# Kernel tuning notes

Hardware: AMD Instinct MI355X
Metric: run time of the kernel (lower is better)

## Reference

```python
import jax, jax.numpy as jnp
import numpy as np

H, C = 33, 16  # heads, out_channels (concat=False -> mean over heads)
NEG_SLOPE = 0.2


def setup_inputs() -> dict:
    key = jax.random.key(0)
    ks = jax.random.split(key, 6)
    N, E, F_in = 50000, 320000, 128
    x = jax.random.normal(ks[0], (N, F_in), dtype=jnp.float32)
    edge_index = jax.random.randint(ks[1], (2, E), 0, N, dtype=jnp.int64)
    W = jax.random.normal(ks[2], (F_in, H * C), dtype=jnp.float32) * (1.0 / np.sqrt(F_in))
    att_src = jax.random.normal(ks[3], (H, C), dtype=jnp.float32) * 0.1
    att_dst = jax.random.normal(ks[4], (H, C), dtype=jnp.float32) * 0.1
    bias = jnp.zeros((C,), dtype=jnp.float32)
    return {"x": x, "edge_index": edge_index, "W": W, "att_src": att_src, "att_dst": att_dst, "bias": bias}


def reference(x, edge_index, W, att_src, att_dst, bias):
    N = x.shape[0]
    # add self loops (PyG GATConv default add_self_loops=True)
    loop = jnp.arange(N, dtype=edge_index.dtype)
    src = jnp.concatenate([edge_index[0], loop])  # [Et]
    dst = jnp.concatenate([edge_index[1], loop])  # [Et]

    h = (x @ W).reshape(N, H, C)                       # [N,H,C]
    a_src = jnp.einsum('nhc,hc->nh', h, att_src)       # [N,H]
    a_dst = jnp.einsum('nhc,hc->nh', h, att_dst)       # [N,H]

    e = a_src[src] + a_dst[dst]                        # [Et,H]
    e = jnp.where(e > 0, e, NEG_SLOPE * e)             # leaky_relu

    # segment softmax over incoming edges of each destination node
    m = jax.ops.segment_max(e, dst, num_segments=N)    # [N,H]
    ex = jnp.exp(e - m[dst])                           # [Et,H]
    denom = jax.ops.segment_sum(ex, dst, num_segments=N)  # [N,H]
    alpha = ex / (denom[dst] + 1e-16)                  # [Et,H]

    msg = alpha[:, :, None] * h[src]                   # [Et,H,C]
    out = jax.ops.segment_sum(msg, dst, num_segments=N)  # [N,H,C]
    out = out.mean(axis=1) + bias                      # concat=False -> mean heads
    return jnp.tanh(out)
```

## Files before the change

kernel.cpp:

```cpp
#include <hip/hip_runtime.h>
#include <math.h>

#define H_HEADS 33
#define C_CH    16
#define HC      528
#define JG      11
#define JGT     13
#define F_IN    128
#define NEG_SLOPE 0.2f

#define BSH   7
#define BMAX  1024
#define PCH   4096

typedef short  bf16x8  __attribute__((ext_vector_type(8)));
typedef float  floatx4 __attribute__((ext_vector_type(4)));

__device__ inline unsigned short f2bf(float f) {
    unsigned int u = __float_as_uint(f);
    unsigned int r = u + 0x7fffu + ((u >> 16) & 1u);
    return (unsigned short)(r >> 16);
}
__device__ inline float bflo(unsigned int u) {
    return __uint_as_float(u << 16);
}
__device__ inline float bfhi(unsigned int u) {
    return __uint_as_float(u & 0xffff0000u);
}

__device__ inline void load_edges4(const int* __restrict__ ei, int E, int Et,
                                   int e0, int* src, int* dst)
{
    if (e0 + 3 < E) {
        int4 s4 = *(const int4*)&ei[e0];
        src[0] = s4.x; src[1] = s4.y; src[2] = s4.z; src[3] = s4.w;
        if ((E & 3) == 0) {
            int4 d4 = *(const int4*)&ei[E + e0];
            dst[0] = d4.x; dst[1] = d4.y; dst[2] = d4.z; dst[3] = d4.w;
        } else {
            #pragma unroll
            for (int k = 0; k < 4; ++k) dst[k] = ei[E + e0 + k];
        }
    } else {
        #pragma unroll
        for (int k = 0; k < 4; ++k) {
            int g = e0 + k;
            if (g < E)       { src[k] = ei[g]; dst[k] = ei[E + g]; }
            else if (g < Et) { src[k] = dst[k] = g - E; }
            else             { src[k] = dst[k] = -1; }
        }
    }
}

#define PW1 (F_IN * HC)
#define PW2 (PW1 + 96 * F_IN)
__global__ void prep_kernel(const float* __restrict__ W,
                            const float* __restrict__ att_src,
                            const float* __restrict__ att_dst,
                            unsigned short* __restrict__ Wt,
                            float4* __restrict__ zout, int nzo,
                            int4* __restrict__ zb, int nzb)
{
    int g = blockIdx.x * blockDim.x + threadIdx.x;
    if (g < PW1) {
        int k = g / HC, n = g % HC;
        Wt[n * F_IN + k] = f2bf(W[g]);
    } else if (g < PW2) {
        int gg = g - PW1;
        int nl = gg >> 7, k = gg & 127;
        int grp = nl / 48, h = nl % 48;
        float v = 0.f;
        if (h < H_HEADS) {
            const float* att = grp ? att_dst : att_src;
            const float* wr  = W + (size_t)k * HC + h * C_CH;
            #pragma unroll
            for (int c = 0; c < C_CH; ++c) v += wr[c] * att[h * C_CH + c];
        }
        Wt[(size_t)(HC + nl) * F_IN + k] = f2bf(v);
    } else {
        int z = g - PW2;
        if (z < nzo)            zout[z]     = make_float4(0.f, 0.f, 0.f, 0.f);
        else if (z - nzo < nzb) zb[z - nzo] = make_int4(0, 0, 0, 0);
    }
}

#define LDA 136
__global__ __launch_bounds__(256) void gemm_att_kernel(
    const float* __restrict__ x, const unsigned short* __restrict__ Wt,
    unsigned short* __restrict__ hb,
    float* __restrict__ a_src, float* __restrict__ a_dstc, int N)
{
    __shared__ unsigned short U[64 * LDA];
    unsigned short (*As)[LDA] = (unsigned short (*)[LDA])U;
    unsigned short (*Bs)[LDA] = (unsigned short (*)[LDA])U;

    const int tid  = threadIdx.x;
    const int lane = tid & 63;
    const int wave = tid >> 6;
    const int lm   = lane & 15;
    const int kc   = lane >> 4;
    const int m0   = blockIdx.x * 64;
    const size_t segN = (size_t)N * 48;

    for (int e = tid; e < 64 * 32; e += 256) {
        int r = e >> 5, c = e & 31;
        int gr = m0 + r;
        float4 v = (gr < N) ? ((const float4*)(x + (size_t)gr * F_IN))[c]
                            : make_float4(0.f, 0.f, 0.f, 0.f);
        unsigned int lo = (unsigned int)f2bf(v.x) | ((unsigned int)f2bf(v.y) << 16);
        unsigned int hi = (unsigned int)f2bf(v.z) | ((unsigned int)f2bf(v.w) << 16);
        *(uint2*)&As[r][c * 4] = make_uint2(lo, hi);
    }

    const uint4* wp = (const uint4*)Wt;
    uint4 rb0 = wp[tid], rb1 = wp[tid + 256], rb2 = wp[tid + 512];

    __syncthreads();

    const int arow = wave * 16 + lm;
    bf16x8 afrag[4];
    #pragma unroll
    for (int ks = 0; ks < 4; ++ks)
        afrag[ks] = *(const bf16x8*)&As[arow][ks * 32 + kc * 8];

    #pragma unroll 1
    for (int j = 0; j < JGT; ++j) {
        __syncthreads();
        *(uint4*)&Bs[tid >> 4][(tid & 15) * 8] = rb0;
        { int e = tid + 256; *(uint4*)&Bs[e >> 4][(e & 15) * 8] = rb1; }
        { int e = tid + 512; *(uint4*)&Bs[e >> 4][(e & 15) * 8] = rb2; }
        if (j + 1 < JGT) {
            int b = (j + 1) * 768;
            rb0 = wp[b + tid]; rb1 = wp[b + tid + 256]; rb2 = wp[b + tid + 512];
        }
        __syncthreads();

        floatx4 acc[3] = {};
        #pragma unroll
        for (int ks = 0; ks < 4; ++ks) {
            #pragma unroll
            for (int t = 0; t < 3; ++t) {
                bf16x8 b = *(const bf16x8*)&Bs[t * 16 + lm][ks * 32 + kc * 8];
                acc[t] = __builtin_amdgcn_mfma_f32_16x16x32_bf16(afrag[ks], b, acc[t], 0, 0, 0);
            }
        }

        #pragma unroll
        for (int t = 0; t < 3; ++t) {
            #pragma unroll
            for (int rr = 0; rr < 4; ++rr) {
                const int row = m0 + wave * 16 + kc * 4 + rr;
                if (row >= N) continue;
                if (j < JG) {
                    hb[(size_t)j * segN + (size_t)row * 48 + t * 16 + lm] =
                        f2bf(acc[t][rr]);
                } else {
                    const int col = t * 16 + lm;
                    if (col < H_HEADS) {
                        float* dstp = (j == JG) ? a_src : a_dstc;
                        dstp[(size_t)row * H_HEADS + col] = acc[t][rr];
                    }
                }
            }
        }
    }
}

__global__ __launch_bounds__(256) void bhist_kernel(const int* __restrict__ ei,
                                                    int* __restrict__ bhist,
                                                    int E, int Et)
{
    __shared__ int lh[2 * BMAX];
    const int tid = threadIdx.x;
    for (int i = tid; i < 2 * BMAX; i += 256) lh[i] = 0;
    __syncthreads();
    int e0 = (blockIdx.x * 256 + tid) * 8;
    if (e0 < Et) {
        int s4[4], d4[4];
        #pragma unroll
        for (int h = 0; h < 2; ++h) {
            load_edges4(ei, E, Et, e0 + h * 4, s4, d4);
            #pragma unroll
            for (int k = 0; k < 4; ++k)
                if (s4[k] >= 0) {
                    atomicAdd(&lh[s4[k] >> BSH], 1);
                    atomicAdd(&lh[BMAX + (d4[k] >> BSH)], 1);
                }
        }
    }
    __syncthreads();
    for (int i = tid; i < 2 * BMAX; i += 256) {
        int v = lh[i];
        if (v) atomicAdd(&bhist[i], v);
    }
}

__global__ __launch_bounds__(1024) void scanb_kernel(const int* __restrict__ bhist,
                                                     int* __restrict__ bbase,
                                                     int* __restrict__ cursor,
                                                     int nb)
{
    const int side = blockIdx.x;
    const int tid  = threadIdx.x;
    const int* h = bhist + side * BMAX;
    int* bb  = bbase  + side * (BMAX + 1);
    int* cur = cursor + side * BMAX;
    __shared__ int sa[1024];
    int v = (tid < nb) ? h[tid] : 0;
    sa[tid] = v;
    __syncthreads();
    for (int off = 1; off < 1024; off <<= 1) {
        int t = (tid >= off) ? sa[tid - off] : 0;
        __syncthreads();
        sa[tid] += t;
        __syncthreads();
    }
    int incl = sa[tid];
    if (tid < nb) {
        bb[tid]  = incl - v;
        cur[tid] = incl - v;
        if (tid == nb - 1) bb[nb] = incl;
    }
}

__global__ __launch_bounds__(256) void part_kernel(const int* __restrict__ ei,
                                                   int* __restrict__ cursor,
                                                   int2* __restrict__ Ag,
                                                   int E, int Et)
{
    __shared__ int2 kv[PCH];
    __shared__ int  lhist[512];
    __shared__ int  gbias[512];
    __shared__ int  wsum[4];
    __shared__ int  sTot;

    const int side = blockIdx.y;
    const int tid  = threadIdx.x;
    const int lane = tid & 63, wid = tid >> 6;
    for (int i = tid; i < 512; i += 256) lhist[i] = 0;
    __syncthreads();

    const int c0 = blockIdx.x * PCH;
    int2 kvr[16];
    #pragma unroll
    for (int r = 0; r < 4; ++r) {
        int e0 = c0 + r * 1024 + tid * 4;
        int s4[4], d4[4];
        load_edges4(ei, E, Et, e0, s4, d4);
        #pragma unroll
        for (int k = 0; k < 4; ++k) {
            int key = side ? d4[k] : s4[k];
            int val = side ? s4[k] : d4[k];
            kvr[r * 4 + k] = make_int2(key, val);
            if (key >= 0) atomicAdd(&lhist[key >> BSH], 1);
        }
    }
    __syncthreads();

    int a0 = lhist[2 * tid], a1 = lhist[2 * tid + 1];
    int pair = a0 + a1, s = pair;
    #pragma unroll
    for (int d = 1; d < 64; d <<= 1) {
        int t = __shfl_up(s, d);
        if (lane >= d) s += t;
    }
    if (lane == 63) wsum[wid] = s;
    __syncthreads();
    if (tid == 0) {
        int run = 0;
        #pragma unroll
        for (int i = 0; i < 4; ++i) { int t = wsum[i]; wsum[i] = run; run += t; }
    }
    __syncthreads();
    int exclT = s - pair + wsum[wid];
    int e0x = exclT, e1x = exclT + a0;
    if (tid == 255) sTot = e1x + a1;
    lhist[2 * tid]     = e0x;
    lhist[2 * tid + 1] = e1x;
    if (a0 > 0) {
        int gb = atomicAdd(&cursor[side * BMAX + 2 * tid], a0);
        gbias[2 * tid] = gb - e0x;
    }
    if (a1 > 0) {
        int gb = atomicAdd(&cursor[side * BMAX + 2 * tid + 1], a1);
        gbias[2 * tid + 1] = gb - e1x;
    }
    __syncthreads();

    #pragma unroll
    for (int k = 0; k < 16; ++k) {
        int key = kvr[k].x;
        if (key >= 0) {
            int lp = atomicAdd(&lhist[key >> BSH], 1);
            kv[lp] = kvr[k];
        }
    }
    __syncthreads();

    const int tot = sTot;
    for (int i = tid; i < tot; i += 256) {
        int2 e = kv[i];
        int b = e.x >> BSH;
        Ag[(size_t)side * Et + gbias[b] + i] = e;
    }
}

__global__ __launch_bounds__(256) void p2_kernel(const int2* __restrict__ Ag,
                                                 const int* __restrict__ bbase,
                                                 int2* __restrict__ e2,
                                                 int* __restrict__ ss2,
                                                 int* __restrict__ off_d,
                                                 int N, int Et, int nb)
{
    const int side = blockIdx.y;
    const int b    = blockIdx.x;
    if (b >= nb) return;
    const int tid  = threadIdx.x;
    const int base = bbase[side * (BMAX + 1) + b];
    const int end  = bbase[side * (BMAX + 1) + b + 1];
    const int k0   = b << BSH;
    const int2* A  = Ag + (size_t)side * Et;

    __shared__ int lh[128];
    __shared__ int w0;
    if (tid < 128) lh[tid] = 0;
    __syncthreads();
    for (int i = base + tid; i < end; i += 256)
        atomicAdd(&lh[A[i].x - k0], 1);
    __syncthreads();

    int v = 0, s = 0;
    if (tid < 128) {
        v = lh[tid]; s = v;
        #pragma unroll
        for (int d = 1; d < 64; d <<= 1) {
            int t = __shfl_up(s, d);
            if ((tid & 63) >= d) s += t;
        }
    }
    if (tid == 63) w0 = s;
    __syncthreads();
    if (tid >= 64 && tid < 128) s += w0;
    int start = base + s - v;
    if (tid < 128) {
        lh[tid] = start;
        if (side == 1 && (k0 + tid) < N) off_d[k0 + tid] = start;
    }
    __syncthreads();

    for (int i = base + tid; i < end; i += 256) {
        int2 e = A[i];
        int pos = atomicAdd(&lh[e.x - k0], 1);
        if (side == 0) e2[pos] = e;
        else           ss2[pos] = e.y;
    }
}

__global__ __launch_bounds__(256) void denom_kernel(
    const int* __restrict__ off_d, const int* __restrict__ ss2,
    const float* __restrict__ a_src, const float* __restrict__ a_dstc,
    float* __restrict__ ad2, int N, int Et)
{
    int g = blockIdx.x * blockDim.x + threadIdx.x;
    if (g >= N * H_HEADS) return;
    const int d = g / H_HEADS, h = g - d * H_HEADS;
    const int beg = off_d[d];
    const int end = (d + 1 < N) ? off_d[d + 1] : Et;
    const float ad = a_dstc[g];
    float acc = 0.f;
    int e = beg;
    for (; e + 4 <= end; e += 4) {
        int s0 = ss2[e], s1 = ss2[e + 1], s2 = ss2[e + 2], s3 = ss2[e + 3];
        float v0 = a_src[(size_t)s0 * H_HEADS + h];
        float v1 = a_src[(size_t)s1 * H_HEADS + h];
        float v2 = a_src[(size_t)s2 * H_HEADS + h];
        float v3 = a_src[(size_t)s3 * H_HEADS + h];
        v0 += ad; v0 = v0 > 0.f ? v0 : NEG_SLOPE * v0;
        v1 += ad; v1 = v1 > 0.f ? v1 : NEG_SLOPE * v1;
        v2 += ad; v2 = v2 > 0.f ? v2 : NEG_SLOPE * v2;
        v3 += ad; v3 = v3 > 0.f ? v3 : NEG_SLOPE * v3;
        acc += __expf(v0);
        acc += __expf(v1);
        acc += __expf(v2);
        acc += __expf(v3);
    }
    for (; e < end; ++e) {
        float v = a_src[(size_t)ss2[e] * H_HEADS + h] + ad;
        v = v > 0.f ? v : NEG_SLOPE * v;
        acc += __expf(v);
    }
    ((float2*)ad2)[g] = make_float2(ad, 1.0f / (acc + 1e-16f));
}

#define EPB 64
__global__ __launch_bounds__(256, 4) void aggregate_kernel(
    const int2* __restrict__ e2,
    const float* __restrict__ a_src, const float* __restrict__ ad2,
    const unsigned short* __restrict__ hb,
    float* __restrict__ out, int N, int Et)
{
    __shared__ int   s_src[EPB], s_dst[EPB];
    __shared__ float s_alpha[EPB][H_HEADS];

    const int nwg = gridDim.x;
    const int q = nwg >> 3, r = nwg & 7;
    const int xcd = blockIdx.x & 7, idx = blockIdx.x >> 3;
    const int bid = (xcd < r ? xcd * (q + 1) : r * (q + 1) + (xcd - r) * q) + idx;

    const int tid = threadIdx.x;
    const int e0  = bid * EPB;
    const size_t segN = (size_t)N * 48;

    if (tid < EPB) {
        int e = e0 + tid;
        int2 v = (e < Et) ? e2[e] : make_int2(0, 0);
        s_src[tid] = v.x; s_dst[tid] = v.y;
    }
    __syncthreads();

    float2 di[9]; float as[9];
    #pragma unroll
    for (int rr = 0; rr < 8; ++rr) {
        int i = tid + rr * 256;
        int el = i / H_HEADS, hd = i - el * H_HEADS;
        di[rr] = ((const float2*)ad2)[(size_t)s_dst[el] * H_HEADS + hd];
        as[rr] = a_src[(size_t)s_src[el] * H_HEADS + hd];
    }
    if (tid < 64) {
        int i = 2048 + tid;
        int el = i / H_HEADS, hd = i - el * H_HEADS;
        di[8] = ((const float2*)ad2)[(size_t)s_dst[el] * H_HEADS + hd];
        as[8] = a_src[(size_t)s_src[el] * H_HEADS + hd];
    }
    __builtin_amdgcn_sched_barrier(0);
    #pragma unroll
    for (int rr = 0; rr < 8; ++rr) {
        int i = tid + rr * 256;
        int el = i / H_HEADS, hd = i - el * H_HEADS;
        float v = as[rr] + di[rr].x;
        v = v > 0.f ? v : NEG_SLOPE * v;
        s_alpha[el][hd] = __expf(v) * di[rr].y;
    }
    if (tid < 64) {
        int i = 2048 + tid;
        int el = i / H_HEADS, hd = i - el * H_HEADS;
        float v = as[8] + di[8].x;
        v = v > 0.f ? v : NEG_SLOPE * v;
        s_alpha[el][hd] = __expf(v) * di[8].y;
    }
    __syncthreads();

    const int el = tid >> 2, cq = tid & 3;
    const int src = s_src[el];
    const unsigned short* hp = hb + (size_t)src * 48 + cq * 4;
    uint2 w[33];
    #pragma unroll
    for (int j = 0; j < JG; ++j) {
        const unsigned short* pj = hp + (size_t)j * segN;
        w[3 * j + 0] = *(const uint2*)(pj);
        w[3 * j + 1] = *(const uint2*)(pj + 16);
        w[3 * j + 2] = *(const uint2*)(pj + 32);
    }
    __builtin_amdgcn_sched_barrier(0);
    float a0 = 0.f, a1 = 0.f, a2 = 0.f, a3 = 0.f;
    #pragma unroll
    for (int j = 0; j < JG; ++j) {
        float l0 = s_alpha[el][3 * j + 0];
        float l1 = s_alpha[el][3 * j + 1];
        float l2 = s_alpha[el][3 * j + 2];
        a0 += l0 * bflo(w[3*j].x) + l1 * bflo(w[3*j+1].x) + l2 * bflo(w[3*j+2].x);
        a1 += l0 * bfhi(w[3*j].x) + l1 * bfhi(w[3*j+1].x) + l2 * bfhi(w[3*j+2].x);
        a2 += l0 * bflo(w[3*j].y) + l1 * bflo(w[3*j+1].y) + l2 * bflo(w[3*j+2].y);
        a3 += l0 * bfhi(w[3*j].y) + l1 * bfhi(w[3*j+1].y) + l2 * bfhi(w[3*j+2].y);
    }

    const int lane  = tid & 63;
    const int wbase = (tid >> 6) * 16;
    #pragma unroll
    for (int qx = 0; qx < 4; ++qx) {
        int S = 16 * qx + ((lane >> 4) << 2) + ((lane & 15) >> 2);
        float s0 = __shfl(a0, S), s1 = __shfl(a1, S);
        float s2 = __shfl(a2, S), s3 = __shfl(a3, S);
        float v = (lane & 2) ? ((lane & 1) ? s3 : s2)
                             : ((lane & 1) ? s1 : s0);
        int elT = wbase + qx * 4 + (lane >> 4);
        if (e0 + elT < Et)
            atomicAdd(&out[s_dst[elT] * C_CH + (lane & 15)], v);
    }
}

__global__ void finalize_kernel(float* __restrict__ out,
                                const float* __restrict__ bias, int total)
{
    int g = blockIdx.x * blockDim.x + threadIdx.x;
    if (g >= total) return;
    out[g] = tanhf(out[g] * (1.0f / 33.0f) + bias[g & 15]);
}

extern "C" void kernel_launch(void* const* d_in, const int* in_sizes, int n_in,
                              void* d_out, int out_size, void* d_ws, size_t ws_size,
                              hipStream_t stream)
{
    const float* x       = (const float*)d_in[0];
    const int*   ei      = (const int*)  d_in[1];
    const float* W       = (const float*)d_in[2];
    const float* att_src = (const float*)d_in[3];
    const float* att_dst = (const float*)d_in[4];
    const float* bias    = (const float*)d_in[5];
    float* out = (float*)d_out;

    const int N  = in_sizes[0] / F_IN;
    const int E  = in_sizes[1] / 2;
    const int Et = E + N;
    const int nb = (N + 127) >> BSH;

    unsigned short* hb = (unsigned short*)d_ws;
    float* a_src  = (float*)(hb + (size_t)N * HC);
    float* a_dstc = a_src + (size_t)N * H_HEADS;
    float* ad2    = a_dstc + (size_t)N * H_HEADS;
    int2*  e2     = (int2*)(ad2 + (size_t)N * 66);
    int*   ss2    = (int*)(e2 + Et);
    int*   off_d  = ss2 + Et;
    int2*  Ag     = (int2*)(off_d + N);
    int*   bhist  = (int*)(Ag + 2 * (size_t)Et);
    int*   bbase  = bhist + 2 * BMAX;
    int*   cursor = bbase + 2 * (BMAX + 1);
    unsigned short* Wt = (unsigned short*)(cursor + 2 * BMAX);

    const int nzo = out_size / 4;
    const int nzb = (2 * BMAX) / 4;
    const int prepTot = PW2 + nzo + nzb;
    prep_kernel<<<(prepTot + 255) / 256, 256, 0, stream>>>(
        W, att_src, att_dst, Wt, (float4*)out, nzo, (int4*)bhist, nzb);

    gemm_att_kernel<<<(N + 63) / 64, 256, 0, stream>>>(x, Wt, hb, a_src, a_dstc, N);

    bhist_kernel<<<(Et + 2047) / 2048, 256, 0, stream>>>(ei, bhist, E, Et);
    scanb_kernel<<<2, 1024, 0, stream>>>(bhist, bbase, cursor, nb);
    part_kernel<<<dim3((Et + PCH - 1) / PCH, 2), 256, 0, stream>>>(
        ei, cursor, Ag, E, Et);
    p2_kernel<<<dim3(nb, 2), 256, 0, stream>>>(Ag, bbase, e2, ss2, off_d,
                                               N, Et, nb);

    denom_kernel<<<(N * H_HEADS + 255) / 256, 256, 0, stream>>>(
        off_d, ss2, a_src, a_dstc, ad2, N, Et);

    aggregate_kernel<<<(Et + EPB - 1) / EPB, 256, 0, stream>>>(
        e2, a_src, ad2, hb, out, N, Et);

    int totO = N * C_CH;
    finalize_kernel<<<(totO + 255) / 256, 256, 0, stream>>>(out, bias, totO);
}
```

Before: 193.4 us.

## Fuse bucket histogram into prep and softmax denominator into p2 sort

Moves the edge bucket histogram into the prep kernel, using global atomics instead of shared-memory histograms, and zeroes the histogram with a memset. Folds the per-destination softmax denominator computation into the p2 counting-sort kernel, reading sorted source ids from LDS when the bucket fits, which drops the off_d array and two kernel launches. Also rewrites the aggregate accumulation with 2-wide float vectors to encourage packed FMA. Trade-offs: global atomics on 2048 bins suffer heavy contention, and denom work now runs on only nb blocks with 256 threads each, so there is less parallelism than the old N*33-thread kernel.

Result: slower. 370.7 us (+91.7%).

```diff
diff --git a/kernel.cpp b/kernel.cpp
--- a/kernel.cpp
+++ b/kernel.cpp
@@ -12,9 +12,11 @@
 #define BSH   7
 #define BMAX  1024
 #define PCH   4096
+#define DCAP  3072
 
 typedef short  bf16x8  __attribute__((ext_vector_type(8)));
 typedef float  floatx4 __attribute__((ext_vector_type(4)));
+typedef float  floatx2 __attribute__((ext_vector_type(2)));
 
 __device__ inline unsigned short f2bf(float f) {
     unsigned int u = __float_as_uint(f);
@@ -59,7 +61,8 @@
                             const float* __restrict__ att_dst,
                             unsigned short* __restrict__ Wt,
                             float4* __restrict__ zout, int nzo,
-                            int4* __restrict__ zb, int nzb)
+                            const int* __restrict__ ei,
+                            int* __restrict__ bhist, int E, int Et)
 {
     int g = blockIdx.x * blockDim.x + threadIdx.x;
     if (g < PW1) {
@@ -79,8 +82,21 @@
         Wt[(size_t)(HC + nl) * F_IN + k] = f2bf(v);
     } else {
         int z = g - PW2;
-        if (z < nzo)            zout[z]     = make_float4(0.f, 0.f, 0.f, 0.f);
-        else if (z - nzo < nzb) zb[z - nzo] = make_int4(0, 0, 0, 0);
+        if (z < nzo) {
+            zout[z] = make_float4(0.f, 0.f, 0.f, 0.f);
+        } else {
+            int e0 = (z - nzo) * 4;
+            if (e0 < Et) {
+                int s4[4], d4[4];
+                load_edges4(ei, E, Et, e0, s4, d4);
+                #pragma unroll
+                for (int k = 0; k < 4; ++k)
+                    if (s4[k] >= 0) {
+                        atomicAdd(&bhist[s4[k] >> BSH], 1);
+                        atomicAdd(&bhist[BMAX + (d4[k] >> BSH)], 1);
+                    }
+            }
+        }
     }
 }
 
@@ -166,35 +182,6 @@
     }
 }
 
-__global__ __launch_bounds__(256) void bhist_kernel(const int* __restrict__ ei,
-                                                    int* __restrict__ bhist,
-                                                    int E, int Et)
-{
-    __shared__ int lh[2 * BMAX];
-    const int tid = threadIdx.x;
-    for (int i = tid; i < 2 * BMAX; i += 256) lh[i] = 0;
-    __syncthreads();
-    int e0 = (blockIdx.x * 256 + tid) * 8;
-    if (e0 < Et) {
-        int s4[4], d4[4];
-        #pragma unroll
-        for (int h = 0; h < 2; ++h) {
-            load_edges4(ei, E, Et, e0 + h * 4, s4, d4);
-            #pragma unroll
-            for (int k = 0; k < 4; ++k)
-                if (s4[k] >= 0) {
-                    atomicAdd(&lh[s4[k] >> BSH], 1);
-                    atomicAdd(&lh[BMAX + (d4[k] >> BSH)], 1);
-                }
-        }
-    }
-    __syncthreads();
-    for (int i = tid; i < 2 * BMAX; i += 256) {
-        int v = lh[i];
-        if (v) atomicAdd(&bhist[i], v);
-    }
-}
-
 __global__ __launch_bounds__(1024) void scanb_kernel(const int* __restrict__ bhist,
                                                      int* __restrict__ bbase,
                                                      int* __restrict__ cursor,
@@ -309,7 +296,9 @@
                                                  const int* __restrict__ bbase,
                                                  int2* __restrict__ e2,
                                                  int* __restrict__ ss2,
-                                                 int* __restrict__ off_d,
+                                                 const float* __restrict__ a_src,
+                                                 const float* __restrict__ a_dstc,
+                                                 float* __restrict__ ad2,
                                                  int N, int Et, int nb)
 {
     const int side = blockIdx.y;
@@ -322,7 +311,9 @@
     const int2* A  = Ag + (size_t)side * Et;
 
     __shared__ int lh[128];
-    __shared__ int w0;
+    __shared__ int st[128];
+    __shared__ int kvlds[DCAP];
+    __shared__ int w0s;
     if (tid < 128) lh[tid] = 0;
     __syncthreads();
     for (int i = base + tid; i < end; i += 256)
@@ -338,58 +329,66 @@
             if ((tid & 63) >= d) s += t;
         }
     }
-    if (tid == 63) w0 = s;
-    __syncthreads();
-    if (tid >= 64 && tid < 128) s += w0;
+    if (tid == 63) w0s = s;
+    __syncthreads();
+    if (tid >= 64 && tid < 128) s += w0s;
     int start = base + s - v;
-    if (tid < 128) {
-        lh[tid] = start;
-        if (side == 1 && (k0 + tid) < N) off_d[k0 + tid] = start;
-    }
-    __syncthreads();
-
+    if (tid < 128) { st[tid] = start; lh[tid] = start; }
+    __syncthreads();
+
+    const int cnt = end - base;
     for (int i = base + tid; i < end; i += 256) {
         int2 e = A[i];
         int pos = atomicAdd(&lh[e.x - k0], 1);
         if (side == 0) e2[pos] = e;
-        else           ss2[pos] = e.y;
-    }
-}
-
-__global__ __launch_bounds__(256) void denom_kernel(
-    const int* __restrict__ off_d, const int* __restrict__ ss2,
-    const float* __restrict__ a_src, const float* __restrict__ a_dstc,
-    float* __restrict__ ad2, int N, int Et)
-{
-    int g = blockIdx.x * blockDim.x + threadIdx.x;
-    if (g >= N * H_HEADS) return;
-    const int d = g / H_HEADS, h = g - d * H_HEADS;
-    const int beg = off_d[d];
-    const int end = (d + 1 < N) ? off_d[d + 1] : Et;
-    const float ad = a_dstc[g];
-    float acc = 0.f;
-    int e = beg;
-    for (; e + 4 <= end; e += 4) {
-        int s0 = ss2[e], s1 = ss2[e + 1], s2 = ss2[e + 2], s3 = ss2[e + 3];
-        float v0 = a_src[(size_t)s0 * H_HEADS + h];
-        float v1 = a_src[(size_t)s1 * H_HEADS + h];
-        float v2 = a_src[(size_t)s2 * H_HEADS + h];
-        float v3 = a_src[(size_t)s3 * H_HEADS + h];
-        v0 += ad; v0 = v0 > 0.f ? v0 : NEG_SLOPE * v0;
-        v1 += ad; v1 = v1 > 0.f ? v1 : NEG_SLOPE * v1;
-        v2 += ad; v2 = v2 > 0.f ? v2 : NEG_SLOPE * v2;
-        v3 += ad; v3 = v3 > 0.f ? v3 : NEG_SLOPE * v3;
-        acc += __expf(v0);
-        acc += __expf(v1);
-        acc += __expf(v2);
-        acc += __expf(v3);
-    }
-    for (; e < end; ++e) {
-        float v = a_src[(size_t)ss2[e] * H_HEADS + h] + ad;
-        v = v > 0.f ? v : NEG_SLOPE * v;
-        acc += __expf(v);
-    }
-    ((float2*)ad2)[g] = make_float2(ad, 1.0f / (acc + 1e-16f));
+        else {
+            ss2[pos] = e.y;
+            int l = pos - base;
+            if (l < DCAP) kvlds[l] = e.y;
+        }
+    }
+    if (side == 0) return;
+    __syncthreads();
+
+    const bool lds_ok = (cnt <= DCAP);
+    for (int p = tid; p < 128 * H_HEADS; p += 256) {
+        int il = p / H_HEADS, h = p - il * H_HEADS;
+        int id = k0 + il;
+        if (id >= N) break;
+        int b0 = st[il], b1 = lh[il];
+        size_t g = (size_t)id * H_HEADS + h;
+        float ad = a_dstc[g];
+        float acc = 0.f;
+        int e = b0;
+        if (lds_ok) {
+            for (; e + 4 <= b1; e += 4) {
+                int s0 = kvlds[e - base],     s1 = kvlds[e - base + 1];
+                int s2 = kvlds[e - base + 2], s3 = kvlds[e - base + 3];
+                float v0 = a_src[(size_t)s0 * H_HEADS + h];
+                float v1 = a_src[(size_t)s1 * H_HEADS + h];
+                float v2 = a_src[(size_t)s2 * H_HEADS + h];
+                float v3 = a_src[(size_t)s3 * H_HEADS + h];
+                v0 += ad; v0 = v0 > 0.f ? v0 : NEG_SLOPE * v0;
+                v1 += ad; v1 = v1 > 0.f ? v1 : NEG_SLOPE * v1;
+                v2 += ad; v2 = v2 > 0.f ? v2 : NEG_SLOPE * v2;
+                v3 += ad; v3 = v3 > 0.f ? v3 : NEG_SLOPE * v3;
+                acc += __expf(v0); acc += __expf(v1);
+                acc += __expf(v2); acc += __expf(v3);
+            }
+            for (; e < b1; ++e) {
+                float vv = a_src[(size_t)kvlds[e - base] * H_HEADS + h] + ad;
+                vv = vv > 0.f ? vv : NEG_SLOPE * vv;
+                acc += __expf(vv);
+            }
+        } else {
+            for (; e < b1; ++e) {
+                float vv = a_src[(size_t)ss2[e] * H_HEADS + h] + ad;
+                vv = vv > 0.f ? vv : NEG_SLOPE * vv;
+                acc += __expf(vv);
+            }
+        }
+        ((float2*)ad2)[g] = make_float2(ad, 1.0f / (acc + 1e-16f));
+    }
 }
 
 #define EPB 64
@@ -462,17 +461,23 @@
         w[3 * j + 2] = *(const uint2*)(pj + 32);
     }
     __builtin_amdgcn_sched_barrier(0);
-    float a0 = 0.f, a1 = 0.f, a2 = 0.f, a3 = 0.f;
+    floatx2 acc01 = {0.f, 0.f}, acc23 = {0.f, 0.f};
     #pragma unroll
     for (int j = 0; j < JG; ++j) {
         float l0 = s_alpha[el][3 * j + 0];
         float l1 = s_alpha[el][3 * j + 1];
         float l2 = s_alpha[el][3 * j + 2];
-        a0 += l0 * bflo(w[3*j].x) + l1 * bflo(w[3*j+1].x) + l2 * bflo(w[3*j+2].x);
-        a1 += l0 * bfhi(w[3*j].x) + l1 * bfhi(w[3*j+1].x) + l2 * bfhi(w[3*j+2].x);
-        a2 += l0 * bflo(w[3*j].y) + l1 * bflo(w[3*j+1].y) + l2 * bflo(w[3*j+2].y);
-        a3 += l0 * bfhi(w[3*j].y) + l1 * bfhi(w[3*j+1].y) + l2 * bfhi(w[3*j+2].y);
-    }
+        uint2 wA = w[3 * j], wB = w[3 * j + 1], wC = w[3 * j + 2];
+        floatx2 hA0 = {bflo(wA.x), bfhi(wA.x)};
+        floatx2 hB0 = {bflo(wB.x), bfhi(wB.x)};
+        floatx2 hC0 = {bflo(wC.x), bfhi(wC.x)};
+        floatx2 hA1 = {bflo(wA.y), bfhi(wA.y)};
+        floatx2 hB1 = {bflo(wB.y), bfhi(wB.y)};
+        floatx2 hC1 = {bflo(wC.y), bfhi(wC.y)};
+        acc01 += hA0 * l0 + hB0 * l1 + hC0 * l2;
+        acc23 += hA1 * l0 + hB1 * l1 + hC1 * l2;
+    }
+    float a0 = acc01.x, a1 = acc01.y, a2 = acc23.x, a3 = acc23.y;
 
     const int lane  = tid & 63;
     const int wbase = (tid >> 6) * 16;
@@ -520,30 +525,27 @@
     float* ad2    = a_dstc + (size_t)N * H_HEADS;
     int2*  e2     = (int2*)(ad2 + (size_t)N * 66);
     int*   ss2    = (int*)(e2 + Et);
-    int*   off_d  = ss2 + Et;
-    int2*  Ag     = (int2*)(off_d + N);
+    int2*  Ag     = (int2*)(ss2 + Et);
     int*   bhist  = (int*)(Ag + 2 * (size_t)Et);
     int*   bbase  = bhist + 2 * BMAX;
     int*   cursor = bbase + 2 * (BMAX + 1);
     unsigned short* Wt = (unsigned short*)(cursor + 2 * BMAX);
 
+    hipMemsetAsync(bhist, 0, 2 * BMAX * sizeof(int), stream);
+
     const int nzo = out_size / 4;
-    const int nzb = (2 * BMAX) / 4;
-    const int prepTot = PW2 + nzo + nzb;
+    const int EtC = (Et + 3) / 4;
+    const int prepTot = PW2 + nzo + EtC;
     prep_kernel<<<(prepTot + 255) / 256, 256, 0, stream>>>(
-        W, att_src, att_dst, Wt, (float4*)out, nzo, (int4*)bhist, nzb);
+        W, att_src, att_dst, Wt, (float4*)out, nzo, ei, bhist, E, Et);
 
     gemm_att_kernel<<<(N + 63) / 64, 256, 0, stream>>>(x, Wt, hb, a_src, a_dstc, N);
 
-    bhist_kernel<<<(Et + 2047) / 2048, 256, 0, stream>>>(ei, bhist, E, Et);
     scanb_kernel<<<2, 1024, 0, stream>>>(bhist, bbase, cursor, nb);
     part_kernel<<<dim3((Et + PCH - 1) / PCH, 2), 256, 0, stream>>>(
         ei, cursor, Ag, E, Et);
-    p2_kernel<<<dim3(nb, 2), 256, 0, stream>>>(Ag, bbase, e2, ss2, off_d,
-                                               N, Et, nb);
-
-    denom_kernel<<<(N * H_HEADS + 255) / 256, 256, 0, stream>>>(
-        off_d, ss2, a_src, a_dstc, ad2, N, Et);
+    p2_kernel<<<dim3(nb, 2), 256, 0, stream>>>(Ag, bbase, e2, ss2,
+                                               a_src, a_dstc, ad2, N, Et, nb);
 
     aggregate_kernel<<<(Et + EPB - 1) / EPB, 256, 0, stream>>>(
         e2, a_src, ad2, hb, out, N, Et);
```

## Stage shared source rows in LDS for aggregation and use packed float2 math

Applied to the files above, without the earlier changes.

The aggregate kernel now detects runs of consecutive edges that share a source node (edges are sorted by source). It stages up to 20 unique source rows of h into shared memory with wide 16-byte loads and makes the per-edge gather read from LDS. Edges beyond the run cap fall back to global loads. Accumulation is rewritten on float2 vectors so the compiler can emit packed FMA, and the bhist zeroing moves from the prep kernel to a hipMemsetAsync call. With random edges most runs are one edge long, so the staging mostly adds LDS traffic, a barrier and about 21 KB of LDS per block, which may lower occupancy.

New measurement: 188.8 us. -2.4%, faster.

```diff
diff --git a/kernel.cpp b/kernel.cpp
--- a/kernel.cpp
+++ b/kernel.cpp
@@ -15,6 +15,7 @@
 
 typedef short  bf16x8  __attribute__((ext_vector_type(8)));
 typedef float  floatx4 __attribute__((ext_vector_type(4)));
+typedef float  floatx2 __attribute__((ext_vector_type(2)));
 
 __device__ inline unsigned short f2bf(float f) {
     unsigned int u = __float_as_uint(f);
@@ -58,8 +59,7 @@
                             const float* __restrict__ att_src,
                             const float* __restrict__ att_dst,
                             unsigned short* __restrict__ Wt,
-                            float4* __restrict__ zout, int nzo,
-                            int4* __restrict__ zb, int nzb)
+                            float4* __restrict__ zout, int nzo)
 {
     int g = blockIdx.x * blockDim.x + threadIdx.x;
     if (g < PW1) {
@@ -79,8 +79,7 @@
         Wt[(size_t)(HC + nl) * F_IN + k] = f2bf(v);
     } else {
         int z = g - PW2;
-        if (z < nzo)            zout[z]     = make_float4(0.f, 0.f, 0.f, 0.f);
-        else if (z - nzo < nzb) zb[z - nzo] = make_int4(0, 0, 0, 0);
+        if (z < nzo) zout[z] = make_float4(0.f, 0.f, 0.f, 0.f);
     }
 }
 
@@ -322,7 +321,7 @@
     const int2* A  = Ag + (size_t)side * Et;
 
     __shared__ int lh[128];
-    __shared__ int w0;
+    __shared__ int w0s;
     if (tid < 128) lh[tid] = 0;
     __syncthreads();
     for (int i = base + tid; i < end; i += 256)
@@ -338,9 +337,9 @@
             if ((tid & 63) >= d) s += t;
         }
     }
-    if (tid == 63) w0 = s;
-    __syncthreads();
-    if (tid >= 64 && tid < 128) s += w0;
+    if (tid == 63) w0s = s;
+    __syncthreads();
+    if (tid >= 64 && tid < 128) s += w0s;
     int start = base + s - v;
     if (tid < 128) {
         lh[tid] = start;
@@ -379,10 +378,8 @@
         v1 += ad; v1 = v1 > 0.f ? v1 : NEG_SLOPE * v1;
         v2 += ad; v2 = v2 > 0.f ? v2 : NEG_SLOPE * v2;
         v3 += ad; v3 = v3 > 0.f ? v3 : NEG_SLOPE * v3;
-        acc += __expf(v0);
-        acc += __expf(v1);
-        acc += __expf(v2);
-        acc += __expf(v3);
+        acc += __expf(v0); acc += __expf(v1);
+        acc += __expf(v2); acc += __expf(v3);
     }
     for (; e < end; ++e) {
         float v = a_src[(size_t)ss2[e] * H_HEADS + h] + ad;
@@ -392,7 +389,9 @@
     ((float2*)ad2)[g] = make_float2(ad, 1.0f / (acc + 1e-16f));
 }
 
-#define EPB 64
+#define EPB  64
+#define RCAP 20
+#define RSTR 536
 __global__ __launch_bounds__(256, 4) void aggregate_kernel(
     const int2* __restrict__ e2,
     const float* __restrict__ a_src, const float* __restrict__ ad2,
@@ -401,6 +400,10 @@
 {
     __shared__ int   s_src[EPB], s_dst[EPB];
     __shared__ float s_alpha[EPB][H_HEADS];
+    __shared__ int   s_ridx[EPB];
+    __shared__ int   s_rowsrc[RCAP];
+    __shared__ int   s_U;
+    __shared__ __align__(16) unsigned short Hrow[RCAP * RSTR];
 
     const int nwg = gridDim.x;
     const int q = nwg >> 3, r = nwg & 7;
@@ -417,6 +420,27 @@
         s_src[tid] = v.x; s_dst[tid] = v.y;
     }
     __syncthreads();
+
+    if (tid < 64) {
+        int src = s_src[tid];
+        bool flag = (tid == 0) || (src != s_src[tid - 1]);
+        unsigned long long b = __ballot(flag);
+        int cntb = __popcll(b & ((1ull << tid) - 1));
+        int run  = flag ? cntb : cntb - 1;
+        s_ridx[tid] = (run < RCAP) ? run : -1;
+        if (flag && run < RCAP) s_rowsrc[run] = src;
+        if (tid == 63) s_U = __popcll(b);
+    }
+    __syncthreads();
+
+    int Un = s_U; if (Un > RCAP) Un = RCAP;
+    for (int i = tid; i < Un * 66; i += 256) {
+        int rr = i / 66, c = i - rr * 66;
+        int j = c / 6, qq = c - j * 6;
+        int srcr = s_rowsrc[rr];
+        uint4 v = *(const uint4*)(hb + (size_t)j * segN + (size_t)srcr * 48 + qq * 8);
+        *(uint4*)&Hrow[rr * RSTR + j * 48 + qq * 8] = v;
+    }
 
     float2 di[9]; float as[9];
     #pragma unroll
@@ -451,28 +475,49 @@
     __syncthreads();
 
     const int el = tid >> 2, cq = tid & 3;
-    const int src = s_src[el];
-    const unsigned short* hp = hb + (size_t)src * 48 + cq * 4;
-    uint2 w[33];
-    #pragma unroll
-    for (int j = 0; j < JG; ++j) {
-        const unsigned short* pj = hp + (size_t)j * segN;
-        w[3 * j + 0] = *(const uint2*)(pj);
-        w[3 * j + 1] = *(const uint2*)(pj + 16);
-        w[3 * j + 2] = *(const uint2*)(pj + 32);
-    }
-    __builtin_amdgcn_sched_barrier(0);
-    float a0 = 0.f, a1 = 0.f, a2 = 0.f, a3 = 0.f;
-    #pragma unroll
-    for (int j = 0; j < JG; ++j) {
-        float l0 = s_alpha[el][3 * j + 0];
-        float l1 = s_alpha[el][3 * j + 1];
-        float l2 = s_alpha[el][3 * j + 2];
-        a0 += l0 * bflo(w[3*j].x) + l1 * bflo(w[3*j+1].x) + l2 * bflo(w[3*j+2].x);
-        a1 += l0 * bfhi(w[3*j].x) + l1 * bfhi(w[3*j+1].x) + l2 * bfhi(w[3*j+2].x);
-        a2 += l0 * bflo(w[3*j].y) + l1 * bflo(w[3*j+1].y) + l2 * bflo(w[3*j+2].y);
-        a3 += l0 * bfhi(w[3*j].y) + l1 * bfhi(w[3*j+1].y) + l2 * bfhi(w[3*j+2].y);
-    }
+    const int rid = s_ridx[el];
+    floatx2 acc01 = {0.f, 0.f}, acc23 = {0.f, 0.f};
+    if (rid >= 0) {
+        const unsigned short* pr = &Hrow[rid * RSTR + cq * 4];
+        #pragma unroll
+        for (int j = 0; j < JG; ++j) {
+            uint2 wA = *(const uint2*)(pr + j * 48);
+            uint2 wB = *(const uint2*)(pr + j * 48 + 16);
+            uint2 wC = *(const uint2*)(pr + j * 48 + 32);
+            float l0 = s_alpha[el][3 * j + 0];
+            float l1 = s_alpha[el][3 * j + 1];
+            float l2 = s_alpha[el][3 * j + 2];
+            floatx2 hA0 = {bflo(wA.x), bfhi(wA.x)};
+            floatx2 hB0 = {bflo(wB.x), bfhi(wB.x)};
+            floatx2 hC0 = {bflo(wC.x), bfhi(wC.x)};
+            floatx2 hA1 = {bflo(wA.y), bfhi(wA.y)};
+            floatx2 hB1 = {bflo(wB.y), bfhi(wB.y)};
+            floatx2 hC1 = {bflo(wC.y), bfhi(wC.y)};
+            acc01 += hA0 * l0 + hB0 * l1 + hC0 * l2;
+            acc23 += hA1 * l0 + hB1 * l1 + hC1 * l2;
+        }
+    } else {
+        const unsigned short* hp = hb + (size_t)s_src[el] * 48 + cq * 4;
+        #pragma unroll
+        for (int j = 0; j < JG; ++j) {
+            const unsigned short* pj = hp + (size_t)j * segN;
+            uint2 wA = *(const uint2*)(pj);
+            uint2 wB = *(const uint2*)(pj + 16);
+            uint2 wC = *(const uint2*)(pj + 32);
+            float l0 = s_alpha[el][3 * j + 0];
+            float l1 = s_alpha[el][3 * j + 1];
+            float l2 = s_alpha[el][3 * j + 2];
+            floatx2 hA0 = {bflo(wA.x), bfhi(wA.x)};
+            floatx2 hB0 = {bflo(wB.x), bfhi(wB.x)};
+            floatx2 hC0 = {bflo(wC.x), bfhi(wC.x)};
+            floatx2 hA1 = {bflo(wA.y), bfhi(wA.y)};
+            floatx2 hB1 = {bflo(wB.y), bfhi(wB.y)};
+            floatx2 hC1 = {bflo(wC.y), bfhi(wC.y)};
+            acc01 += hA0 * l0 + hB0 * l1 + hC0 * l2;
+            acc23 += hA1 * l0 + hB1 * l1 + hC1 * l2;
+        }
+    }
+    float a0 = acc01.x, a1 = acc01.y, a2 = acc23.x, a3 = acc23.y;
 
     const int lane  = tid & 63;
     const int wbase = (tid >> 6) * 16;
@@ -527,11 +572,12 @@
     int*   cursor = bbase + 2 * (BMAX + 1);
     unsigned short* Wt = (unsigned short*)(cursor + 2 * BMAX);
 
+    hipMemsetAsync(bhist, 0, 2 * BMAX * sizeof(int), stream);
+
     const int nzo = out_size / 4;
-    const int nzb = (2 * BMAX) / 4;
-    const int prepTot = PW2 + nzo + nzb;
+    const int prepTot = PW2 + nzo;
     prep_kernel<<<(prepTot + 255) / 256, 256, 0, stream>>>(
-        W, att_src, att_dst, Wt, (float4*)out, nzo, (int4*)bhist, nzb);
+        W, att_src, att_dst, Wt, (float4*)out, nzo);
 
     gemm_att_kernel<<<(N + 63) / 64, 256, 0, stream>>>(x, Wt, hb, a_src, a_dstc, N);
 
```
